# Performance work log

Hardware: AMD Instinct MI355X
Metric: run time of the kernel (lower is better)

## Reference

```python
import jax, jax.numpy as jnp
import numpy as np

N = 400_000   # units (atoms)
C = 4         # n_channel
A = 3         # n_axis
D = 128       # d_hidden
NBLK = 50_000 # blocks
B = 64        # batches (static segment count)
NR = 16       # n_rbf
CUT = 7.0     # cutoff
LN_EPS = 1e-5


def radial_basis(d):
    # GemNet-style: polynomial envelope (exponent 5) * Gaussian basis on d/cutoff
    ds = d / CUT
    env = 1.0 - 21.0 * ds**5 + 35.0 * ds**6 - 15.0 * ds**7
    env = jnp.where(ds < 1.0, env, 0.0)
    offsets = jnp.linspace(0.0, 1.0, NR)
    coeff = -0.5 / (offsets[1] - offsets[0]) ** 2
    g = jnp.exp(coeff * (ds[:, None] - offsets[None, :]) ** 2)  # [M, NR]
    return env[:, None] * g


def setup_inputs() -> dict:
    key = jax.random.key(0)
    ks = jax.random.split(key, 8)
    H = jax.random.normal(ks[0], (N, D), jnp.float32)
    Z = jax.random.normal(ks[1], (N, C, A), jnp.float32)
    block_id = jnp.sort(jax.random.randint(ks[2], (N,), 0, NBLK))
    batch_id = jnp.sort(jax.random.randint(ks[3], (NBLK,), 0, B))
    sigma = jnp.ones((1, C, 1), jnp.float32)
    W1 = jax.random.normal(ks[4], (C * NR, D), jnp.float32) / np.sqrt(C * NR)
    b1 = jnp.zeros((D,), jnp.float32)
    W2 = jax.random.normal(ks[5], (D, D), jnp.float32) / np.sqrt(D)
    b2 = jnp.zeros((D,), jnp.float32)
    ln_w = jnp.ones((D,), jnp.float32)
    ln_b = jnp.zeros((D,), jnp.float32)
    return {"H": H, "Z": Z, "sigma": sigma, "W1": W1, "b1": b1, "W2": W2,
            "b2": b2, "ln_w": ln_w, "ln_b": ln_b,
            "block_id": block_id, "batch_id": batch_id}


def reference(H, Z, sigma, W1, b1, W2, b2, ln_w, ln_b, block_id, batch_id):
    uid = batch_id[block_id]                                  # [N]
    cnt = jax.ops.segment_sum(jnp.ones((N,), jnp.float32), uid, num_segments=B)
    cnt_safe = jnp.maximum(cnt, 1.0)

    # scatter_mean(Z, uid) -> per-batch centroid [B, C, A]
    Zsum = jax.ops.segment_sum(Z.reshape(N, C * A), uid, num_segments=B)
    Z_c = (Zsum / cnt_safe[:, None]).reshape(B, C, A)
    Z_cg = Z_c[uid]                                           # [N, C, A]
    Z_cent = Z - Z_cg

    # scatter_std over (units x axes) per channel, unbiased
    src = jnp.swapaxes(Z_cent, 1, 2).reshape(N * A, C)        # [N*A, C]
    idx3 = jnp.repeat(uid, A)                                 # [N*A]
    cnt3 = cnt * A
    mean_s = jax.ops.segment_sum(src, idx3, num_segments=B) / jnp.maximum(cnt3, 1.0)[:, None]
    sq = jax.ops.segment_sum((src - mean_s[idx3]) ** 2, idx3, num_segments=B)
    var = sq / jnp.maximum(cnt3 - 1.0, 1.0)[:, None]
    std = jnp.sqrt(var)                                       # [B, C]

    rescale = (1.0 / std)[:, :, None] * sigma                 # [B, C, 1]
    Z_out = Z_cg + Z_cent * rescale[uid]

    rbf = radial_basis(rescale.reshape(-1)).reshape(B, C * NR)  # [B, C*NR]
    h = jax.nn.silu(rbf @ W1 + b1)
    h = jax.nn.silu(h @ W2 + b2)                              # [B, D]

    Hn = H + h[uid]
    mu = jnp.mean(Hn, axis=-1, keepdims=True)
    v = jnp.var(Hn, axis=-1, keepdims=True)
    H_out = (Hn - mu) * jax.lax.rsqrt(v + LN_EPS) * ln_w + ln_b
    return (H_out, Z_out, rescale)
```

## Files before the change

### kernel.cpp

```cpp
#include <hip/hip_runtime.h>
#include <hip/hip_bf16.h>

#define N_ATOMS 400000
#define N_BLOCKS 50000
#define BATCHES 64
#define CCH 4
#define AX 3
#define DH 128
#define NRBF 16

#define ACC_OFF 0
#define ZC_OFF  1088
#define RS_OFF  1856
#define HB_OFF  2112
#define UID_OFF 10304

typedef float f4 __attribute__((ext_vector_type(4)));

__device__ __forceinline__ f4 ntload4(const f4* p) { return __builtin_nontemporal_load(p); }
__device__ __forceinline__ void ntstore4(f4* p, f4 v) { __builtin_nontemporal_store(v, p); }
__device__ __forceinline__ float silu_f(float x) { return x / (1.f + expf(-x)); }

__global__ __launch_bounds__(256) void k1_stats(
    const float* __restrict__ Z, const int* __restrict__ block_id,
    const int* __restrict__ batch_id, float* __restrict__ acc,
    unsigned char* __restrict__ uid8) {
  __shared__ float bins[BATCHES * 17];
  for (int i = threadIdx.x; i < BATCHES * 17; i += 256) bins[i] = 0.f;
  __syncthreads();

  const f4* Z4 = (const f4*)Z;
  int n = blockIdx.x * 256 + threadIdx.x;
  bool valid = (n < N_ATOMS);
  int uid = -1;
  float z[12];
#pragma unroll
  for (int j = 0; j < 12; ++j) z[j] = 0.f;
  if (valid) {
    uid = batch_id[block_id[n]];
    uid8[n] = (unsigned char)uid;
    f4 a = Z4[n * 3 + 0];
    f4 b = Z4[n * 3 + 1];
    f4 c = Z4[n * 3 + 2];
    z[0] = a.x; z[1] = a.y; z[2]  = a.z; z[3]  = a.w;
    z[4] = b.x; z[5] = b.y; z[6]  = b.z; z[7]  = b.w;
    z[8] = c.x; z[9] = c.y; z[10] = c.z; z[11] = c.w;
  }

  int lo = valid ? uid : 0x7fffffff;
  int hi = uid;
#pragma unroll
  for (int m = 32; m; m >>= 1) {
    lo = min(lo, __shfl_xor(lo, m));
    hi = max(hi, __shfl_xor(hi, m));
  }

  if (lo == hi) {
    float vals[16];
#pragma unroll
    for (int j = 0; j < 12; ++j) vals[j] = z[j];
#pragma unroll
    for (int c = 0; c < 4; ++c)
      vals[12 + c] = z[c*3]*z[c*3] + z[c*3+1]*z[c*3+1] + z[c*3+2]*z[c*3+2];
#pragma unroll
    for (int v = 0; v < 16; ++v) {
      float x = vals[v];
#pragma unroll
      for (int m = 32; m; m >>= 1) x += __shfl_xor(x, m);
      vals[v] = x;
    }
    unsigned long long mb = __ballot(valid);
    if ((threadIdx.x & 63) == 0) {
      atomicAdd(&bins[hi * 17 + 0], (float)__popcll(mb));
#pragma unroll
      for (int v = 0; v < 16; ++v) atomicAdd(&bins[hi * 17 + 1 + v], vals[v]);
    }
  } else if (hi >= 0) {
    if (valid) {
      atomicAdd(&bins[uid * 17 + 0], 1.f);
#pragma unroll
      for (int j = 0; j < 12; ++j) atomicAdd(&bins[uid * 17 + 1 + j], z[j]);
#pragma unroll
      for (int c = 0; c < 4; ++c)
        atomicAdd(&bins[uid * 17 + 13 + c],
                  z[c*3]*z[c*3] + z[c*3+1]*z[c*3+1] + z[c*3+2]*z[c*3+2]);
    }
  }
  __syncthreads();
  for (int i = threadIdx.x; i < BATCHES * 17; i += 256) {
    float v = bins[i];
    if (v != 0.f) atomicAdd(&acc[i], v);
  }
}

__global__ __launch_bounds__(128) void k2_mlp(
    const float* __restrict__ sigma, const float* __restrict__ W1,
    const float* __restrict__ b1, const float* __restrict__ W2,
    const float* __restrict__ b2, const float* __restrict__ acc,
    float* __restrict__ Zc, float* __restrict__ resc,
    float* __restrict__ hbuf, float* __restrict__ resc_out) {
  int b = blockIdx.x, t = threadIdx.x;
  __shared__ float rbf_s[64];
  __shared__ float h1_s[128];
  __shared__ float resc_s[4];

  if (t < 4) {
    int c = t;
    float cnt = acc[b * 17];
    float cs = fmaxf(cnt, 1.f);
    float s2 = 0.f;
#pragma unroll
    for (int a = 0; a < 3; ++a) {
      float zc = acc[b * 17 + 1 + c * 3 + a] / cs;
      Zc[b * 12 + c * 3 + a] = zc;
      s2 += zc * zc;
    }
    float sq = acc[b * 17 + 13 + c] - cnt * s2;
    float denom = fmaxf(cnt * 3.f - 1.f, 1.f);
    float var = fmaxf(sq / denom, 0.f);
    float r = sigma[c] / sqrtf(var);
    resc_s[c] = r;
    resc[b * 4 + c] = r;
    resc_out[b * 4 + c] = r;
  }
  __syncthreads();
  if (t < 64) {
    int c = t >> 4, ri = t & 15;
    float ds = resc_s[c] * (1.f / 7.f);
    float env = 0.f;
    if (ds < 1.f) {
      float d2 = ds * ds;
      float d5 = d2 * d2 * ds;
      env = 1.f - 21.f * d5 + 35.f * d5 * ds - 15.f * d5 * d2;
    }
    float off = (float)ri * (1.f / 15.f);
    float dd = ds - off;
    rbf_s[t] = env * expf(-112.5f * dd * dd);
  }
  __syncthreads();
  float s = b1[t];
#pragma unroll 8
  for (int k = 0; k < 64; ++k) s += rbf_s[k] * W1[k * 128 + t];
  h1_s[t] = silu_f(s);
  __syncthreads();
  float s2 = b2[t];
#pragma unroll 8
  for (int k = 0; k < 128; ++k) s2 += h1_s[k] * W2[k * 128 + t];
  hbuf[b * 128 + t] = silu_f(s2);
}

__global__ __launch_bounds__(256) void k3_apply(
    const float* __restrict__ H, const float* __restrict__ Z,
    const unsigned char* __restrict__ uid8,
    const float* __restrict__ ln_w, const float* __restrict__ ln_b,
    const float* __restrict__ Zc, const float* __restrict__ resc,
    const float* __restrict__ hbuf,
    float* __restrict__ Hout, float* __restrict__ Zout) {
  int t = threadIdx.x;
  int sub = t >> 4, l = t & 15;
  int base = blockIdx.x * 32;
  int n0 = base + sub * 2;
  int n1 = n0 + 1;

  unsigned short u2 = *(const unsigned short*)&uid8[n0];
  int uid0 = u2 & 0xff, uid1 = u2 >> 8;

  const f4* H4 = (const f4*)H;
  const f4* HB4 = (const f4*)hbuf;
  size_t r0 = (size_t)n0 * 32, r1 = (size_t)n1 * 32;
  f4 v00 = ntload4(&H4[r0 + l]);
  f4 v01 = ntload4(&H4[r0 + 16 + l]);
  f4 v10 = ntload4(&H4[r1 + l]);
  f4 v11 = ntload4(&H4[r1 + 16 + l]);
  f4 hb00 = HB4[uid0 * 32 + l];
  f4 hb01 = HB4[uid0 * 32 + 16 + l];
  f4 hb10 = HB4[uid1 * 32 + l];
  f4 hb11 = HB4[uid1 * 32 + 16 + l];

  f4 x00 = v00 + hb00, x01 = v01 + hb01;
  f4 x10 = v10 + hb10, x11 = v11 + hb11;

  float s0 = (x00.x + x00.y + x00.z + x00.w) + (x01.x + x01.y + x01.z + x01.w);
  float q0 = (x00.x*x00.x + x00.y*x00.y + x00.z*x00.z + x00.w*x00.w)
           + (x01.x*x01.x + x01.y*x01.y + x01.z*x01.z + x01.w*x01.w);
  float s1 = (x10.x + x10.y + x10.z + x10.w) + (x11.x + x11.y + x11.z + x11.w);
  float q1 = (x10.x*x10.x + x10.y*x10.y + x10.z*x10.z + x10.w*x10.w)
           + (x11.x*x11.x + x11.y*x11.y + x11.z*x11.z + x11.w*x11.w);
#pragma unroll
  for (int m = 1; m < 16; m <<= 1) {
    s0 += __shfl_xor(s0, m);
    q0 += __shfl_xor(q0, m);
    s1 += __shfl_xor(s1, m);
    q1 += __shfl_xor(q1, m);
  }
  float mean0 = s0 * (1.f / 128.f);
  float inv0 = rsqrtf(q0 * (1.f / 128.f) - mean0 * mean0 + 1e-5f);
  float mean1 = s1 * (1.f / 128.f);
  float inv1 = rsqrtf(q1 * (1.f / 128.f) - mean1 * mean1 + 1e-5f);

  const f4* LW4 = (const f4*)ln_w;
  const f4* LB4 = (const f4*)ln_b;
  f4 w0 = LW4[l], w1 = LW4[16 + l];
  f4 bb0 = LB4[l], bb1 = LB4[16 + l];

  f4 o;
  f4* HO4 = (f4*)Hout;
  o.x = (x00.x - mean0) * inv0 * w0.x + bb0.x;
  o.y = (x00.y - mean0) * inv0 * w0.y + bb0.y;
  o.z = (x00.z - mean0) * inv0 * w0.z + bb0.z;
  o.w = (x00.w - mean0) * inv0 * w0.w + bb0.w;
  ntstore4(&HO4[r0 + l], o);
  o.x = (x01.x - mean0) * inv0 * w1.x + bb1.x;
  o.y = (x01.y - mean0) * inv0 * w1.y + bb1.y;
  o.z = (x01.z - mean0) * inv0 * w1.z + bb1.z;
  o.w = (x01.w - mean0) * inv0 * w1.w + bb1.w;
  ntstore4(&HO4[r0 + 16 + l], o);
  o.x = (x10.x - mean1) * inv1 * w0.x + bb0.x;
  o.y = (x10.y - mean1) * inv1 * w0.y + bb0.y;
  o.z = (x10.z - mean1) * inv1 * w0.z + bb0.z;
  o.w = (x10.w - mean1) * inv1 * w0.w + bb0.w;
  ntstore4(&HO4[r1 + l], o);
  o.x = (x11.x - mean1) * inv1 * w1.x + bb1.x;
  o.y = (x11.y - mean1) * inv1 * w1.y + bb1.y;
  o.z = (x11.z - mean1) * inv1 * w1.z + bb1.z;
  o.w = (x11.w - mean1) * inv1 * w1.w + bb1.w;
  ntstore4(&HO4[r1 + 16 + l], o);

  if (t < 96) {
    int atom = base + t / 3;
    int comp = t - (t / 3) * 3;
    int uid = uid8[atom];
    const f4* Z4 = (const f4*)Z;
    f4 z = Z4[atom * 3 + comp];
    float zz[4] = {z.x, z.y, z.z, z.w};
    float oo[4];
#pragma unroll
    for (int k = 0; k < 4; ++k) {
      int j = comp * 4 + k;
      int c = j / 3;
      float zcv = Zc[uid * 12 + j];
      float r = resc[uid * 4 + c];
      oo[k] = zcv + (zz[k] - zcv) * r;
    }
    f4 ov = {oo[0], oo[1], oo[2], oo[3]};
    ntstore4(&((f4*)Zout)[atom * 3 + comp], ov);
  }
}

extern "C" void kernel_launch(void* const* d_in, const int* in_sizes, int n_in,
                              void* d_out, int out_size, void* d_ws, size_t ws_size,
                              hipStream_t stream) {
  const float* H     = (const float*)d_in[0];
  const float* Z     = (const float*)d_in[1];
  const float* sigma = (const float*)d_in[2];
  const float* W1    = (const float*)d_in[3];
  const float* b1    = (const float*)d_in[4];
  const float* W2    = (const float*)d_in[5];
  const float* b2    = (const float*)d_in[6];
  const float* ln_w  = (const float*)d_in[7];
  const float* ln_b  = (const float*)d_in[8];
  const int* block_id = (const int*)d_in[9];
  const int* batch_id = (const int*)d_in[10];

  float* ws   = (float*)d_ws;
  float* acc  = ws + ACC_OFF;
  float* Zc   = ws + ZC_OFF;
  float* resc = ws + RS_OFF;
  float* hbuf = ws + HB_OFF;
  unsigned char* uid8 = (unsigned char*)(ws + UID_OFF);

  float* Hout = (float*)d_out;
  float* Zout = Hout + (size_t)N_ATOMS * DH;
  float* resc_out = Zout + (size_t)N_ATOMS * CCH * AX;

  hipMemsetAsync(acc, 0, BATCHES * 17 * sizeof(float), stream);
  k1_stats<<<(N_ATOMS + 255) / 256, 256, 0, stream>>>(Z, block_id, batch_id, acc, uid8);
  k2_mlp<<<BATCHES, 128, 0, stream>>>(sigma, W1, b1, W2, b2, acc, Zc, resc, hbuf, resc_out);
  k3_apply<<<N_ATOMS / 32, 256, 0, stream>>>(H, Z, uid8, ln_w, ln_b,
                                             Zc, resc, hbuf, Hout, Zout);
}
```

Before: 106.0 us.

## Fuse per-batch MLP into apply kernel, recomputing it per block

Removes the separate 64-block MLP kernel and its launch. Each apply block now recomputes rescale, centroids and the two-layer MLP for the at most two batch ids its 32 sorted atoms can span. The MLP results are kept in shared memory instead of a global buffer. This saves one launch and one dependency gap, but 12,500 blocks each redo 64x128 plus 128x128 MACs and add three extra barriers before the bandwidth-bound LayerNorm. Correctness also relies on each 32-atom block touching at most two consecutive batches.

```diff
diff --git a/kernel.cpp b/kernel.cpp
--- a/kernel.cpp
+++ b/kernel.cpp
@@ -2,18 +2,11 @@
 #include <hip/hip_bf16.h>
 
 #define N_ATOMS 400000
-#define N_BLOCKS 50000
 #define BATCHES 64
-#define CCH 4
-#define AX 3
 #define DH 128
-#define NRBF 16
 
 #define ACC_OFF 0
-#define ZC_OFF  1088
-#define RS_OFF  1856
-#define HB_OFF  2112
-#define UID_OFF 10304
+#define UID_OFF 2048
 
 typedef float f4 __attribute__((ext_vector_type(4)));
 
@@ -93,40 +86,80 @@
   }
 }
 
-__global__ __launch_bounds__(128) void k2_mlp(
-    const float* __restrict__ sigma, const float* __restrict__ W1,
-    const float* __restrict__ b1, const float* __restrict__ W2,
-    const float* __restrict__ b2, const float* __restrict__ acc,
-    float* __restrict__ Zc, float* __restrict__ resc,
-    float* __restrict__ hbuf, float* __restrict__ resc_out) {
-  int b = blockIdx.x, t = threadIdx.x;
-  __shared__ float rbf_s[64];
-  __shared__ float h1_s[128];
-  __shared__ float resc_s[4];
-
-  if (t < 4) {
-    int c = t;
-    float cnt = acc[b * 17];
+__global__ __launch_bounds__(256) void k3_apply(
+    const float* __restrict__ H, const float* __restrict__ Z,
+    const unsigned char* __restrict__ uid8,
+    const float* __restrict__ sigma,
+    const float* __restrict__ W1, const float* __restrict__ b1,
+    const float* __restrict__ W2, const float* __restrict__ b2,
+    const float* __restrict__ ln_w, const float* __restrict__ ln_b,
+    const float* __restrict__ acc,
+    float* __restrict__ Hout, float* __restrict__ Zout,
+    float* __restrict__ resc_out) {
+  int t = threadIdx.x;
+  int base = blockIdx.x * 32;
+  int sub = t >> 4, l = t & 15;
+  int n0 = base + sub * 2;
+  int n1 = n0 + 1;
+
+  __shared__ float resc_s[2][4];
+  __shared__ float zc_s[2][12];
+  __shared__ float rbf_s[2][64];
+  __shared__ float h1_s[2][128];
+  __shared__ float h_s[2][128];
+  __shared__ int uidlo_s;
+
+  unsigned short u2 = *(const unsigned short*)&uid8[n0];
+  int uid0 = u2 & 0xff, uid1 = u2 >> 8;
+  if (t == 0) uidlo_s = uid0;
+
+  const f4* H4 = (const f4*)H;
+  size_t r0 = (size_t)n0 * 32, r1 = (size_t)n1 * 32;
+  f4 v00 = ntload4(&H4[r0 + l]);
+  f4 v01 = ntload4(&H4[r0 + 16 + l]);
+  f4 v10 = ntload4(&H4[r1 + l]);
+  f4 v11 = ntload4(&H4[r1 + 16 + l]);
+
+  f4 zv = {0.f, 0.f, 0.f, 0.f};
+  int za = 0, zcomp = 0, zuid = 0;
+  if (t < 96) {
+    za = t / 3;
+    zcomp = t - za * 3;
+    zuid = uid8[base + za];
+    zv = ((const f4*)Z)[(base + za) * 3 + zcomp];
+  }
+
+  if (t < 8) {
+    int slot = t >> 2, c = t & 3;
+    int u = uid8[base + (slot ? 31 : 0)];
+    float cnt = acc[u * 17];
     float cs = fmaxf(cnt, 1.f);
     float s2 = 0.f;
 #pragma unroll
     for (int a = 0; a < 3; ++a) {
-      float zc = acc[b * 17 + 1 + c * 3 + a] / cs;
-      Zc[b * 12 + c * 3 + a] = zc;
+      float zc = acc[u * 17 + 1 + c * 3 + a] / cs;
       s2 += zc * zc;
     }
-    float sq = acc[b * 17 + 13 + c] - cnt * s2;
+    float sq = acc[u * 17 + 13 + c] - cnt * s2;
     float denom = fmaxf(cnt * 3.f - 1.f, 1.f);
     float var = fmaxf(sq / denom, 0.f);
     float r = sigma[c] / sqrtf(var);
-    resc_s[c] = r;
-    resc[b * 4 + c] = r;
-    resc_out[b * 4 + c] = r;
-  }
-  __syncthreads();
-  if (t < 64) {
-    int c = t >> 4, ri = t & 15;
-    float ds = resc_s[c] * (1.f / 7.f);
+    resc_s[slot][c] = r;
+    resc_out[u * 4 + c] = r;
+  }
+  if (t >= 32 && t < 56) {
+    int tt = t - 32;
+    int slot = tt / 12, j = tt - slot * 12;
+    int u = uid8[base + (slot ? 31 : 0)];
+    float cs = fmaxf(acc[u * 17], 1.f);
+    zc_s[slot][j] = acc[u * 17 + 1 + j] / cs;
+  }
+  __syncthreads();
+
+  if (t < 128) {
+    int slot = t >> 6, i = t & 63;
+    int c = i >> 4, ri = i & 15;
+    float ds = resc_s[slot][c] * (1.f / 7.f);
     float env = 0.f;
     if (ds < 1.f) {
       float d2 = ds * ds;
@@ -135,68 +168,55 @@
     }
     float off = (float)ri * (1.f / 15.f);
     float dd = ds - off;
-    rbf_s[t] = env * expf(-112.5f * dd * dd);
-  }
-  __syncthreads();
-  float s = b1[t];
+    rbf_s[slot][i] = env * expf(-112.5f * dd * dd);
+  }
+  __syncthreads();
+
+  {
+    int slot = t >> 7, col = t & 127;
+    float s = b1[col];
 #pragma unroll 8
-  for (int k = 0; k < 64; ++k) s += rbf_s[k] * W1[k * 128 + t];
-  h1_s[t] = silu_f(s);
-  __syncthreads();
-  float s2 = b2[t];
+    for (int k = 0; k < 64; ++k) s += rbf_s[slot][k] * W1[k * 128 + col];
+    h1_s[slot][col] = silu_f(s);
+  }
+  __syncthreads();
+
+  {
+    int slot = t >> 7, col = t & 127;
+    float s = b2[col];
 #pragma unroll 8
-  for (int k = 0; k < 128; ++k) s2 += h1_s[k] * W2[k * 128 + t];
-  hbuf[b * 128 + t] = silu_f(s2);
-}
-
-__global__ __launch_bounds__(256) void k3_apply(
-    const float* __restrict__ H, const float* __restrict__ Z,
-    const unsigned char* __restrict__ uid8,
-    const float* __restrict__ ln_w, const float* __restrict__ ln_b,
-    const float* __restrict__ Zc, const float* __restrict__ resc,
-    const float* __restrict__ hbuf,
-    float* __restrict__ Hout, float* __restrict__ Zout) {
-  int t = threadIdx.x;
-  int sub = t >> 4, l = t & 15;
-  int base = blockIdx.x * 32;
-  int n0 = base + sub * 2;
-  int n1 = n0 + 1;
-
-  unsigned short u2 = *(const unsigned short*)&uid8[n0];
-  int uid0 = u2 & 0xff, uid1 = u2 >> 8;
-
-  const f4* H4 = (const f4*)H;
-  const f4* HB4 = (const f4*)hbuf;
-  size_t r0 = (size_t)n0 * 32, r1 = (size_t)n1 * 32;
-  f4 v00 = ntload4(&H4[r0 + l]);
-  f4 v01 = ntload4(&H4[r0 + 16 + l]);
-  f4 v10 = ntload4(&H4[r1 + l]);
-  f4 v11 = ntload4(&H4[r1 + 16 + l]);
-  f4 hb00 = HB4[uid0 * 32 + l];
-  f4 hb01 = HB4[uid0 * 32 + 16 + l];
-  f4 hb10 = HB4[uid1 * 32 + l];
-  f4 hb11 = HB4[uid1 * 32 + 16 + l];
-
-  f4 x00 = v00 + hb00, x01 = v01 + hb01;
-  f4 x10 = v10 + hb10, x11 = v11 + hb11;
-
-  float s0 = (x00.x + x00.y + x00.z + x00.w) + (x01.x + x01.y + x01.z + x01.w);
-  float q0 = (x00.x*x00.x + x00.y*x00.y + x00.z*x00.z + x00.w*x00.w)
-           + (x01.x*x01.x + x01.y*x01.y + x01.z*x01.z + x01.w*x01.w);
-  float s1 = (x10.x + x10.y + x10.z + x10.w) + (x11.x + x11.y + x11.z + x11.w);
-  float q1 = (x10.x*x10.x + x10.y*x10.y + x10.z*x10.z + x10.w*x10.w)
-           + (x11.x*x11.x + x11.y*x11.y + x11.z*x11.z + x11.w*x11.w);
+    for (int k = 0; k < 128; ++k) s += h1_s[slot][k] * W2[k * 128 + col];
+    h_s[slot][col] = silu_f(s);
+  }
+  __syncthreads();
+
+  int uid_lo = uidlo_s;
+  int s0 = min(uid0 - uid_lo, 1);
+  int s1 = min(uid1 - uid_lo, 1);
+  const f4* hs0 = (const f4*)h_s[s0];
+  const f4* hs1 = (const f4*)h_s[s1];
+  f4 x00 = v00 + hs0[l];
+  f4 x01 = v01 + hs0[16 + l];
+  f4 x10 = v10 + hs1[l];
+  f4 x11 = v11 + hs1[16 + l];
+
+  float ss0 = (x00.x + x00.y + x00.z + x00.w) + (x01.x + x01.y + x01.z + x01.w);
+  float qq0 = (x00.x*x00.x + x00.y*x00.y + x00.z*x00.z + x00.w*x00.w)
+            + (x01.x*x01.x + x01.y*x01.y + x01.z*x01.z + x01.w*x01.w);
+  float ss1 = (x10.x + x10.y + x10.z + x10.w) + (x11.x + x11.y + x11.z + x11.w);
+  float qq1 = (x10.x*x10.x + x10.y*x10.y + x10.z*x10.z + x10.w*x10.w)
+            + (x11.x*x11.x + x11.y*x11.y + x11.z*x11.z + x11.w*x11.w);
 #pragma unroll
   for (int m = 1; m < 16; m <<= 1) {
-    s0 += __shfl_xor(s0, m);
-    q0 += __shfl_xor(q0, m);
-    s1 += __shfl_xor(s1, m);
-    q1 += __shfl_xor(q1, m);
-  }
-  float mean0 = s0 * (1.f / 128.f);
-  float inv0 = rsqrtf(q0 * (1.f / 128.f) - mean0 * mean0 + 1e-5f);
-  float mean1 = s1 * (1.f / 128.f);
-  float inv1 = rsqrtf(q1 * (1.f / 128.f) - mean1 * mean1 + 1e-5f);
+    ss0 += __shfl_xor(ss0, m);
+    qq0 += __shfl_xor(qq0, m);
+    ss1 += __shfl_xor(ss1, m);
+    qq1 += __shfl_xor(qq1, m);
+  }
+  float mean0 = ss0 * (1.f / 128.f);
+  float inv0 = rsqrtf(qq0 * (1.f / 128.f) - mean0 * mean0 + 1e-5f);
+  float mean1 = ss1 * (1.f / 128.f);
+  float inv1 = rsqrtf(qq1 * (1.f / 128.f) - mean1 * mean1 + 1e-5f);
 
   const f4* LW4 = (const f4*)ln_w;
   const f4* LB4 = (const f4*)ln_b;
@@ -227,23 +247,19 @@
   ntstore4(&HO4[r1 + 16 + l], o);
 
   if (t < 96) {
-    int atom = base + t / 3;
-    int comp = t - (t / 3) * 3;
-    int uid = uid8[atom];
-    const f4* Z4 = (const f4*)Z;
-    f4 z = Z4[atom * 3 + comp];
-    float zz[4] = {z.x, z.y, z.z, z.w};
+    int sz = min(zuid - uid_lo, 1);
+    float zz[4] = {zv.x, zv.y, zv.z, zv.w};
     float oo[4];
 #pragma unroll
     for (int k = 0; k < 4; ++k) {
-      int j = comp * 4 + k;
+      int j = zcomp * 4 + k;
       int c = j / 3;
-      float zcv = Zc[uid * 12 + j];
-      float r = resc[uid * 4 + c];
+      float zcv = zc_s[sz][j];
+      float r = resc_s[sz][c];
       oo[k] = zcv + (zz[k] - zcv) * r;
     }
     f4 ov = {oo[0], oo[1], oo[2], oo[3]};
-    ntstore4(&((f4*)Zout)[atom * 3 + comp], ov);
+    ntstore4(&((f4*)Zout)[(base + za) * 3 + zcomp], ov);
   }
 }
 
@@ -264,18 +280,14 @@
 
   float* ws   = (float*)d_ws;
   float* acc  = ws + ACC_OFF;
-  float* Zc   = ws + ZC_OFF;
-  float* resc = ws + RS_OFF;
-  float* hbuf = ws + HB_OFF;
   unsigned char* uid8 = (unsigned char*)(ws + UID_OFF);
 
   float* Hout = (float*)d_out;
   float* Zout = Hout + (size_t)N_ATOMS * DH;
-  float* resc_out = Zout + (size_t)N_ATOMS * CCH * AX;
+  float* resc_out = Zout + (size_t)N_ATOMS * 12;
 
   hipMemsetAsync(acc, 0, BATCHES * 17 * sizeof(float), stream);
   k1_stats<<<(N_ATOMS + 255) / 256, 256, 0, stream>>>(Z, block_id, batch_id, acc, uid8);
-  k2_mlp<<<BATCHES, 128, 0, stream>>>(sigma, W1, b1, W2, b2, acc, Zc, resc, hbuf, resc_out);
-  k3_apply<<<N_ATOMS / 32, 256, 0, stream>>>(H, Z, uid8, ln_w, ln_b,
-                                             Zc, resc, hbuf, Hout, Zout);
+  k3_apply<<<N_ATOMS / 32, 256, 0, stream>>>(H, Z, uid8, sigma, W1, b1, W2, b2,
+                                             ln_w, ln_b, acc, Hout, Zout, resc_out);
 }
```

Result: slower. 158.2 us (+49.3%).
